# Optimization experiments

Measured on AMD Instinct MI355X. Metric: run time of the kernel, lower is better.

The kernel has to match this reference:

```python
import jax, jax.numpy as jnp
import numpy as np

N_TF, N_GENES, W, FANIN, B = 1024, 20000, 4, 16, 128
M = N_GENES * W  # middle width = 80000


def _build_edges(rng):
    # layer 1: each of the M per-gene nodes draws FANIN random TF inputs
    out1 = np.repeat(np.arange(M, dtype=np.int32), FANIN)
    in1 = rng.integers(0, N_TF, size=M * FANIN).astype(np.int32)
    in1[-1] = N_TF - 1  # ensure full input dim is touched
    # layer 2: dense WxW block per gene (node i of gene g sees all W nodes of gene g)
    out2 = np.repeat(np.arange(M, dtype=np.int32), W)
    gene = np.arange(M, dtype=np.int32) // W
    in2 = (gene[:, None] * W + np.arange(W, dtype=np.int32)[None, :]).reshape(-1)
    # layer 3: each gene output sums its W nodes
    out3 = np.repeat(np.arange(N_GENES, dtype=np.int32), W)
    in3 = np.arange(M, dtype=np.int32)
    return out1, in1, out2, in2, out3, in3


def setup_inputs() -> dict:
    key = jax.random.key(0)
    ks = jax.random.split(key, 7)
    rng = np.random.default_rng(0)
    out1, in1, out2, in2, out3, in3 = _build_edges(rng)
    scale1 = 1.0 / np.sqrt(FANIN)
    scale2 = 1.0 / np.sqrt(W)
    return {
        "features": jax.random.normal(ks[0], (B, N_TF), jnp.float32),
        "w1": jax.random.normal(ks[1], (out1.shape[0],), jnp.float32) * scale1,
        "b1": jax.random.normal(ks[2], (M,), jnp.float32) * 0.01,
        "w2": jax.random.normal(ks[3], (out2.shape[0],), jnp.float32) * scale2,
        "b2": jax.random.normal(ks[4], (M,), jnp.float32) * 0.01,
        "w3": jax.random.normal(ks[5], (out3.shape[0],), jnp.float32) * scale2,
        "b3": jax.random.normal(ks[6], (N_GENES,), jnp.float32) * 0.01,
        "out1": jnp.asarray(out1), "in1": jnp.asarray(in1),
        "out2": jnp.asarray(out2), "in2": jnp.asarray(in2),
        "out3": jnp.asarray(out3), "in3": jnp.asarray(in3),
    }


def _sparse_linear(x, w, b, out_idx, in_idx):
    # x: [B, n_in]; per-edge gather-multiply-scatter, y[b, o] = sum_e w_e * x[b, in_e] + b_o
    contrib = x.T[in_idx] * w[:, None]                      # [nnz, B]
    y = jax.ops.segment_sum(contrib, out_idx, num_segments=b.shape[0])  # [n_out, B]
    return y.T + b


def reference(features, w1, b1, w2, b2, w3, b3, out1, in1, out2, in2, out3, in3):
    h = jnp.tanh(_sparse_linear(features, w1, b1, out1, in1))
    h = jnp.tanh(_sparse_linear(h, w2, b2, out2, in2))
    return _sparse_linear(h, w3, b3, out3, in3)  # [B, N_GENES]
```

## Files before the change

### kernel.cpp

```cpp
#include <hip/hip_runtime.h>
#include <hip/hip_fp16.h>

#define N_TF    1024
#define N_GENES 20000
#define WW      4
#define FANIN   16
#define BATCH   128
#define EPG     (WW * FANIN)
#define MM      (N_GENES * WW)
#define NNZ1    (N_GENES * EPG)

#define GPB      16
#define NTHREADS 1024
#define NBLK     (N_GENES / GPB)
#define YROW     (BATCH + 2)

typedef unsigned int uint32;

__device__ __forceinline__ float2 fast_tanh2(float a, float b) {
    const float ta = __expf(2.0f * a);
    const float tb = __expf(2.0f * b);
    const float da = ta + 1.0f;
    const float db = tb + 1.0f;
    const float r  = __builtin_amdgcn_rcpf(da * db);
    return make_float2(fmaf(-2.0f * db, r, 1.0f),
                       fmaf(-2.0f * da, r, 1.0f));
}

__device__ __forceinline__ float cvt_ub0(uint32 v) {
#if __has_builtin(__builtin_amdgcn_cvt_f32_ubyte0)
    return __builtin_amdgcn_cvt_f32_ubyte0(v);
#else
    return (float)(v & 0xffu);
#endif
}
__device__ __forceinline__ float cvt_ub1(uint32 v) {
#if __has_builtin(__builtin_amdgcn_cvt_f32_ubyte1)
    return __builtin_amdgcn_cvt_f32_ubyte1(v);
#else
    return (float)((v >> 8) & 0xffu);
#endif
}

__global__ __launch_bounds__(512) void prep1_kernel(
    const float* __restrict__ features,
    unsigned char* __restrict__ xu,
    float2*       __restrict__ so)
{
    const int wid  = threadIdx.x >> 6;
    const int lane = threadIdx.x & 63;
    const int tf   = blockIdx.x * 8 + wid;

    const float a = features[(2 * lane)     * N_TF + tf];
    const float b = features[(2 * lane + 1) * N_TF + tf];
    float mn = fminf(a, b), mx = fmaxf(a, b);
#pragma unroll
    for (int off = 1; off < 64; off <<= 1) {
        mn = fminf(mn, __shfl_xor(mn, off, 64));
        mx = fmaxf(mx, __shfl_xor(mx, off, 64));
    }
    const float range = fmaxf(mx - mn, 1e-20f);
    const float inv   = 255.0f / range;
    const float s     = range * (1.0f / 255.0f);

    float va = fmaf(a - mn, inv, 0.5f);
    float vb = fmaf(b - mn, inv, 0.5f);
    va = fminf(fmaxf(va, 0.0f), 255.0f);
    vb = fminf(fmaxf(vb, 0.0f), 255.0f);
    const uint32 ua = (uint32)va;
    const uint32 ub = (uint32)vb;
    *(unsigned short*)(xu + tf * BATCH + 2 * lane) =
        (unsigned short)(ua | (ub << 8));

    if (lane == 0) so[tf] = make_float2(s, mn);
}

__global__ __launch_bounds__(256) void prep2_kernel(
    const int*    __restrict__ in1,
    const float*  __restrict__ w1,
    const float*  __restrict__ b1,
    const float2* __restrict__ so,
    float*        __restrict__ w1s,
    float*        __restrict__ b1p)
{
    const int n = blockIdx.x * 256 + threadIdx.x;
    if (n >= MM) return;
    float corr = 0.0f;
#pragma unroll
    for (int j = 0; j < FANIN; ++j) {
        const int    e   = n * FANIN + j;
        const int    idx = in1[e];
        const float  w   = w1[e];
        const float2 p   = so[idx];
        w1s[e] = w * p.x;
        corr  = fmaf(w, p.y, corr);
    }
    b1p[n] = b1[n] + corr;
}

__global__ __launch_bounds__(NTHREADS, 4) void fused_kernel(
    const unsigned char* __restrict__ xu,
    const int*    __restrict__ in1,
    const float*  __restrict__ w1s,
    const float*  __restrict__ b1p,
    const float*  __restrict__ w2,
    const float*  __restrict__ b2,
    const float*  __restrict__ w3,
    const float*  __restrict__ b3,
    float*        __restrict__ out)
{
    __shared__ float yt[GPB * YROW];

    const int tid  = threadIdx.x;
    const int wid  = __builtin_amdgcn_readfirstlane(tid >> 6);
    const int lane = tid & 63;
    const int g    = blockIdx.x * GPB + wid;
    const int voff = lane << 1;
    const char* xb = (const char*)xu;

    const uint4*  __restrict__ ig = (const uint4*)(in1 + g * EPG);
    const float4* __restrict__ wg = (const float4*)(w1s + g * EPG);

    float2 acc[WW];
#pragma unroll
    for (int i = 0; i < WW; ++i) acc[i] = make_float2(0.0f, 0.0f);

#pragma unroll
    for (int half = 0; half < 2; ++half) {
        uint32 idx[32];
        float  wsc[32];
#pragma unroll
        for (int k = 0; k < 8; ++k) {
            const uint4  iq = ig[half * 8 + k];
            const float4 wq = wg[half * 8 + k];
            idx[k * 4 + 0] = iq.x;  idx[k * 4 + 1] = iq.y;
            idx[k * 4 + 2] = iq.z;  idx[k * 4 + 3] = iq.w;
            wsc[k * 4 + 0] = wq.x;  wsc[k * 4 + 1] = wq.y;
            wsc[k * 4 + 2] = wq.z;  wsc[k * 4 + 3] = wq.w;
        }
        unsigned short xv[32];
#pragma unroll
        for (int t = 0; t < 32; ++t)
            xv[t] = *(const unsigned short*)(xb + (((size_t)idx[t]) << 7) + voff);
#pragma unroll
        for (int t = 0; t < 32; ++t) {
            const uint32 v  = (uint32)xv[t];
            const float  x0 = cvt_ub0(v);
            const float  x1 = cvt_ub1(v);
            const int tt = half * 32 + t;
            const int nd = tt >> 4;
            acc[nd].x = fmaf(wsc[t], x0, acc[nd].x);
            acc[nd].y = fmaf(wsc[t], x1, acc[nd].y);
        }
    }

    float2 h1[WW];
#pragma unroll
    for (int i = 0; i < WW; ++i) {
        const float bb = b1p[g * WW + i];
        h1[i] = fast_tanh2(acc[i].x + bb, acc[i].y + bb);
    }

    float2 h2[WW];
#pragma unroll
    for (int i = 0; i < WW; ++i) {
        const float4 w  = *(const float4*)(w2 + g * 16 + i * 4);
        const float  bb = b2[g * WW + i];
        const float sx = bb + w.x * h1[0].x + w.y * h1[1].x
                            + w.z * h1[2].x + w.w * h1[3].x;
        const float sy = bb + w.x * h1[0].y + w.y * h1[1].y
                            + w.z * h1[2].y + w.w * h1[3].y;
        h2[i] = fast_tanh2(sx, sy);
    }

    const float4 wv3 = *(const float4*)(w3 + g * 4);
    const float  bv  = b3[g];
    const float yx = bv + wv3.x * h2[0].x + wv3.y * h2[1].x
                        + wv3.z * h2[2].x + wv3.w * h2[3].x;
    const float yy = bv + wv3.x * h2[0].y + wv3.y * h2[1].y
                        + wv3.z * h2[2].y + wv3.w * h2[3].y;

    float2* ytw = (float2*)(yt + wid * YROW);
    ytw[lane] = make_float2(yx, yy);

    __syncthreads();

    const int g0 = blockIdx.x * GPB;
#pragma unroll
    for (int it = 0; it < (BATCH * GPB) / NTHREADS; ++it) {
        const int idx = it * NTHREADS + tid;
        const int gq  = idx & (GPB - 1);
        const int b   = idx >> 4;
        out[b * N_GENES + g0 + gq] = yt[gq * YROW + b];
    }
}

extern "C" void kernel_launch(void* const* d_in, const int* in_sizes, int n_in,
                              void* d_out, int out_size, void* d_ws, size_t ws_size,
                              hipStream_t stream)
{
    const float* features = (const float*)d_in[0];
    const float* w1 = (const float*)d_in[1];
    const float* b1 = (const float*)d_in[2];
    const float* w2 = (const float*)d_in[3];
    const float* b2 = (const float*)d_in[4];
    const float* w3 = (const float*)d_in[5];
    const float* b3 = (const float*)d_in[6];
    const int*   in1 = (const int*)d_in[8];
    float* out = (float*)d_out;

    unsigned char* xu  = (unsigned char*)d_ws;
    float2*        so  = (float2*)((char*)d_ws + (size_t)N_TF * BATCH);
    float*         w1s = (float*)((char*)so + (size_t)N_TF * sizeof(float2));
    float*         b1p = w1s + NNZ1;

    hipLaunchKernelGGL(prep1_kernel, dim3(N_TF / 8), dim3(512), 0, stream,
                       features, xu, so);
    hipLaunchKernelGGL(prep2_kernel, dim3((MM + 255) / 256), dim3(256), 0, stream,
                       in1, w1, b1, so, w1s, b1p);
    hipLaunchKernelGGL(fused_kernel, dim3(NBLK), dim3(NTHREADS), 0, stream,
                       xu, in1, w1s, b1p, w2, b2, w3, b3, out);
}
```

Before: 118.4 us.

## Gather 4 batch bytes per lane, split edges across half-waves and reduce

Each lane now loads a 32-bit word (four batch columns) instead of a 16-bit pair. The two half-waves process alternate edges and are combined with a cross-half shuffle reduction. This halves the number of gather instructions per lane and widens each memory access. In exchange it adds a reduction step, duplicates the tanh and layer-2/3 work across both halves, and pads the LDS row to 132 floats for aligned float4 stores.

Result: slower. 179.9 us (+51.9%).

```diff
diff --git a/kernel.cpp b/kernel.cpp
--- a/kernel.cpp
+++ b/kernel.cpp
@@ -13,7 +13,7 @@
 #define GPB      16
 #define NTHREADS 1024
 #define NBLK     (N_GENES / GPB)
-#define YROW     (BATCH + 2)
+#define YROW     132
 
 typedef unsigned int uint32;
 
@@ -39,6 +39,20 @@
     return __builtin_amdgcn_cvt_f32_ubyte1(v);
 #else
     return (float)((v >> 8) & 0xffu);
+#endif
+}
+__device__ __forceinline__ float cvt_ub2(uint32 v) {
+#if __has_builtin(__builtin_amdgcn_cvt_f32_ubyte2)
+    return __builtin_amdgcn_cvt_f32_ubyte2(v);
+#else
+    return (float)((v >> 16) & 0xffu);
+#endif
+}
+__device__ __forceinline__ float cvt_ub3(uint32 v) {
+#if __has_builtin(__builtin_amdgcn_cvt_f32_ubyte3)
+    return __builtin_amdgcn_cvt_f32_ubyte3(v);
+#else
+    return (float)((v >> 24) & 0xffu);
 #endif
 }
 
@@ -115,15 +129,15 @@
     const int wid  = __builtin_amdgcn_readfirstlane(tid >> 6);
     const int lane = tid & 63;
     const int g    = blockIdx.x * GPB + wid;
-    const int voff = lane << 1;
-    const char* xb = (const char*)xu;
+    const bool odd = (lane & 32) != 0;
+    const uint32 lb = (uint32)((lane & 31) << 2);
 
     const uint4*  __restrict__ ig = (const uint4*)(in1 + g * EPG);
     const float4* __restrict__ wg = (const float4*)(w1s + g * EPG);
 
-    float2 acc[WW];
-#pragma unroll
-    for (int i = 0; i < WW; ++i) acc[i] = make_float2(0.0f, 0.0f);
+    float4 acc[WW];
+#pragma unroll
+    for (int i = 0; i < WW; ++i) acc[i] = make_float4(0.f, 0.f, 0.f, 0.f);
 
 #pragma unroll
     for (int half = 0; half < 2; ++half) {
@@ -138,50 +152,71 @@
             wsc[k * 4 + 0] = wq.x;  wsc[k * 4 + 1] = wq.y;
             wsc[k * 4 + 2] = wq.z;  wsc[k * 4 + 3] = wq.w;
         }
-        unsigned short xv[32];
-#pragma unroll
-        for (int t = 0; t < 32; ++t)
-            xv[t] = *(const unsigned short*)(xb + (((size_t)idx[t]) << 7) + voff);
-#pragma unroll
-        for (int t = 0; t < 32; ++t) {
-            const uint32 v  = (uint32)xv[t];
-            const float  x0 = cvt_ub0(v);
-            const float  x1 = cvt_ub1(v);
-            const int tt = half * 32 + t;
-            const int nd = tt >> 4;
-            acc[nd].x = fmaf(wsc[t], x0, acc[nd].x);
-            acc[nd].y = fmaf(wsc[t], x1, acc[nd].y);
+        uint32 xv[16];
+#pragma unroll
+        for (int p = 0; p < 16; ++p) {
+            const uint32 offA = idx[2 * p]     << 7;
+            const uint32 offB = idx[2 * p + 1] << 7;
+            const uint32 off  = (odd ? offB : offA) + lb;
+            xv[p] = *(const uint32*)(xu + off);
         }
-    }
-
-    float2 h1[WW];
+#pragma unroll
+        for (int p = 0; p < 16; ++p) {
+            const float  w  = odd ? wsc[2 * p + 1] : wsc[2 * p];
+            const uint32 v  = xv[p];
+            const int    nd = (half * 32 + 2 * p) >> 4;
+            acc[nd].x = fmaf(w, cvt_ub0(v), acc[nd].x);
+            acc[nd].y = fmaf(w, cvt_ub1(v), acc[nd].y);
+            acc[nd].z = fmaf(w, cvt_ub2(v), acc[nd].z);
+            acc[nd].w = fmaf(w, cvt_ub3(v), acc[nd].w);
+        }
+    }
+
+#pragma unroll
+    for (int i = 0; i < WW; ++i) {
+        acc[i].x += __shfl_xor(acc[i].x, 32, 64);
+        acc[i].y += __shfl_xor(acc[i].y, 32, 64);
+        acc[i].z += __shfl_xor(acc[i].z, 32, 64);
+        acc[i].w += __shfl_xor(acc[i].w, 32, 64);
+    }
+
+    float4 h1[WW];
 #pragma unroll
     for (int i = 0; i < WW; ++i) {
         const float bb = b1p[g * WW + i];
-        h1[i] = fast_tanh2(acc[i].x + bb, acc[i].y + bb);
-    }
-
-    float2 h2[WW];
+        const float2 t0 = fast_tanh2(acc[i].x + bb, acc[i].y + bb);
+        const float2 t1 = fast_tanh2(acc[i].z + bb, acc[i].w + bb);
+        h1[i] = make_float4(t0.x, t0.y, t1.x, t1.y);
+    }
+
+    float4 h2[WW];
 #pragma unroll
     for (int i = 0; i < WW; ++i) {
         const float4 w  = *(const float4*)(w2 + g * 16 + i * 4);
         const float  bb = b2[g * WW + i];
-        const float sx = bb + w.x * h1[0].x + w.y * h1[1].x
+        const float s0 = bb + w.x * h1[0].x + w.y * h1[1].x
                             + w.z * h1[2].x + w.w * h1[3].x;
-        const float sy = bb + w.x * h1[0].y + w.y * h1[1].y
+        const float s1 = bb + w.x * h1[0].y + w.y * h1[1].y
                             + w.z * h1[2].y + w.w * h1[3].y;
-        h2[i] = fast_tanh2(sx, sy);
+        const float s2 = bb + w.x * h1[0].z + w.y * h1[1].z
+                            + w.z * h1[2].z + w.w * h1[3].z;
+        const float s3 = bb + w.x * h1[0].w + w.y * h1[1].w
+                            + w.z * h1[2].w + w.w * h1[3].w;
+        const float2 t0 = fast_tanh2(s0, s1);
+        const float2 t1 = fast_tanh2(s2, s3);
+        h2[i] = make_float4(t0.x, t0.y, t1.x, t1.y);
     }
 
     const float4 wv3 = *(const float4*)(w3 + g * 4);
     const float  bv  = b3[g];
-    const float yx = bv + wv3.x * h2[0].x + wv3.y * h2[1].x
-                        + wv3.z * h2[2].x + wv3.w * h2[3].x;
-    const float yy = bv + wv3.x * h2[0].y + wv3.y * h2[1].y
-                        + wv3.z * h2[2].y + wv3.w * h2[3].y;
-
-    float2* ytw = (float2*)(yt + wid * YROW);
-    ytw[lane] = make_float2(yx, yy);
+    float4 y;
+    y.x = bv + wv3.x * h2[0].x + wv3.y * h2[1].x + wv3.z * h2[2].x + wv3.w * h2[3].x;
+    y.y = bv + wv3.x * h2[0].y + wv3.y * h2[1].y + wv3.z * h2[2].y + wv3.w * h2[3].y;
+    y.z = bv + wv3.x * h2[0].z + wv3.y * h2[1].z + wv3.z * h2[2].z + wv3.w * h2[3].z;
+    y.w = bv + wv3.x * h2[0].w + wv3.y * h2[1].w + wv3.z * h2[2].w + wv3.w * h2[3].w;
+
+    if (!odd)
+        *(float4*)(yt + wid * YROW + ((lane & 31) << 2)) = y;
 
     __syncthreads();
 
```
